# Kernel tuning notes

Measured on AMD Instinct MI355X. Metric: run time of the kernel, lower is better.

Reference implementation:

```python
import jax, jax.numpy as jnp
import numpy as np

N_NODES = 50000
N_EDGES = 800000
NC = 16
FDIM = 13
FHID = 64


def setup_inputs() -> dict:
    key = jax.random.key(0)
    ks = jax.random.split(key, 10)
    inp = {
        "hx": jax.random.normal(ks[0], (N_NODES, NC), jnp.float32),
        "edgefeats": jax.random.normal(ks[1], (N_EDGES, FDIM), jnp.float32),
        "idxn": jax.random.randint(ks[2], (N_EDGES,), 0, N_NODES, jnp.int32),
        "edge_dst": jnp.sort(jax.random.randint(ks[3], (N_EDGES,), 0, N_NODES, jnp.int32)),
        "fnet_w1": jax.random.normal(ks[4], (FDIM, FHID), jnp.float32) * 0.3,
        "fnet_b1": jnp.zeros((FHID,), jnp.float32),
        "fnet_w2": jax.random.normal(ks[5], (FHID, NC * NC), jnp.float32) * 0.05,
        "fnet_b2": jnp.zeros((NC * NC,), jnp.float32),
        "w_ih": jax.random.normal(ks[6], (3 * NC, NC), jnp.float32) * 0.25,
        "w_hh": jax.random.normal(ks[7], (3 * NC, NC), jnp.float32) * 0.25,
        "b_ih": jnp.zeros((3 * NC,), jnp.float32),
        "b_hh": jnp.zeros((3 * NC,), jnp.float32),
    }
    return inp


def _gru_cell(x, h, w_ih, w_hh, b_ih, b_hh):
    gi = x @ w_ih.T + b_ih  # [N, 3*nc]
    gh = h @ w_hh.T + b_hh
    i_r, i_z, i_n = jnp.split(gi, 3, axis=1)
    h_r, h_z, h_n = jnp.split(gh, 3, axis=1)
    r = jax.nn.sigmoid(i_r + h_r)
    z = jax.nn.sigmoid(i_z + h_z)
    n = jnp.tanh(i_n + r * h_n)
    return (1.0 - z) * n + z * h


def reference(hx, edgefeats, idxn, edge_dst, fnet_w1, fnet_b1, fnet_w2, fnet_b2,
              w_ih, w_hh, b_ih, b_hh):
    n_nodes, nc = hx.shape
    # Filter-generating network: per-edge [nc, nc] weight matrices (shared over iterations).
    w_flat = jax.nn.relu(edgefeats @ fnet_w1 + fnet_b1) @ fnet_w2 + fnet_b2
    W = w_flat.reshape(-1, nc, nc)  # [E, nc, nc]
    # Degree normalization per destination node.
    deg = jax.ops.segment_sum(jnp.ones_like(edge_dst, dtype=hx.dtype), edge_dst,
                              num_segments=n_nodes)
    inv_deg = (1.0 / jnp.maximum(deg, 1.0))[:, None]  # [N, 1]

    def gconv(h):
        msgs = jnp.einsum('ec,ecd->ed', h[idxn], W)  # gather + per-edge matmul
        agg = jax.ops.segment_sum(msgs, edge_dst, num_segments=n_nodes)
        return agg * inv_deg

    def cell(inp, h):
        return _gru_cell(inp, h, w_ih, w_hh, b_ih, b_hh)

    hxs = [hx]
    h1 = cell(gconv(hx), hx); hxs.append(h1)
    h2 = cell(gconv(h1), h1); hxs.append(h2)
    h3 = cell(gconv(h2), h2)
    s1 = h1 + h3; hxs.append(s1)
    h4 = cell(gconv(s1), s1); hxs.append(h4)
    h5 = cell(gconv(h4), h4)
    s2 = h3 + h5; hxs.append(s2)
    h6 = cell(gconv(s2), s2); hxs.append(h6)
    h7 = cell(gconv(h6), h6)
    s3 = h5 + h7; hxs.append(s3)
    h8 = cell(gconv(s3), s3); hxs.append(h8)
    h9 = cell(gconv(h8), h8)
    s4 = h7 + h9; hxs.append(s4)
    h10 = cell(gconv(s4), s4); hxs.append(h10)
    return jnp.concatenate(hxs, axis=1)  # cat_all=True -> [N, 11*nc]
```

## Files before the change

kernel.cpp:

```cpp
#include <hip/hip_runtime.h>

#define NN 50000
#define NE 800000
#define OUTC 176

typedef unsigned int uint32;
typedef short bf16x8 __attribute__((ext_vector_type(8)));
typedef float f32x4 __attribute__((ext_vector_type(4)));

__device__ __forceinline__ uint32 f2bf_rne(float f) {
  union { float f; uint32 u; } v; v.f = f;
  uint32 u = v.u;
  return (u + 0x7FFFu + ((u >> 16) & 1u)) >> 16;
}
__device__ __forceinline__ uint32 packbf2(float a, float b) {
  return f2bf_rne(a) | (f2bf_rne(b) << 16);
}
__device__ __forceinline__ float blo(uint32 u) {
  union { uint32 x; float f; } t; t.x = u << 16; return t.f;
}
__device__ __forceinline__ float bhi(uint32 u) {
  union { uint32 x; float f; } t; t.x = u & 0xFFFF0000u; return t.f;
}
__device__ __forceinline__ float bf2f(unsigned short v) {
  union { uint32 x; float f; } t; t.x = ((uint32)v) << 16; return t.f;
}
__device__ __forceinline__ float sb2f(uint32 w, int b) {
  return (float)((int)(w << (24 - 8 * b)) >> 24);
}

__global__ __launch_bounds__(256) void deg_count_kernel(const int* __restrict__ edst,
                                                        float* __restrict__ deg) {
  int e = blockIdx.x * 256 + threadIdx.x;
  if (e < NE) atomicAdd(&deg[edst[e]], 1.0f);
}

__global__ __launch_bounds__(256) void deg_inv_kernel(float* __restrict__ deg) {
  int n = blockIdx.x * 256 + threadIdx.x;
  if (n < NN) deg[n] = 1.0f / fmaxf(deg[n], 1.0f);
}

__global__ __launch_bounds__(256) void copy_col0_kernel(const float* __restrict__ hx,
                                                        float* __restrict__ out) {
  int n = blockIdx.x * 256 + threadIdx.x;
  if (n >= NN) return;
  const float4* s = reinterpret_cast<const float4*>(hx + (size_t)n * 16);
  float4* d = reinterpret_cast<float4*>(out + (size_t)n * OUTC);
  d[0] = s[0]; d[1] = s[1]; d[2] = s[2]; d[3] = s[3];
}

__global__ __launch_bounds__(256) void repack_w2_kernel(const float* __restrict__ w2,
                                                        float* __restrict__ w2t) {
  int i = blockIdx.x * 256 + threadIdx.x;
  if (i >= 256 * 1024) return;
  int d = i >> 10, r = i & 1023, k = r >> 4, c = r & 15;
  w2t[i] = w2[k * 256 + c * 16 + d];
}

__global__ __launch_bounds__(256) void repack_w2f_kernel(const float* __restrict__ w2,
                                                         unsigned short* __restrict__ w2f) {
  int i = blockIdx.x * 256 + threadIdx.x;
  if (i >= 16384) return;
  int jj = i & 7;
  int l = (i >> 3) & 63;
  int nbm = i >> 9;
  int m = nbm & 1, nb = nbm >> 1;
  int k = m * 32 + (l >> 4) * 8 + jj;
  int j = nb * 16 + (l & 15);
  w2f[i] = (unsigned short)f2bf_rne(w2[k * 256 + j]);
}

__global__ __launch_bounds__(256) void fnet_mfma_i8_kernel(
    const float* __restrict__ ef, const float* __restrict__ w1, const float* __restrict__ b1,
    const unsigned short* __restrict__ w2f, const float* __restrict__ b2,
    unsigned char* __restrict__ W, unsigned short* __restrict__ S, int wo) {
  __shared__ float efs[832];
  const int wave = threadIdx.x >> 6;
  const int l = threadIdx.x & 63;
  const int wid = wo + blockIdx.x * 4 + wave;
  const int d = l & 15, kg = l >> 4;

  long long E0 = ((long long)wo + (long long)blockIdx.x * 4) * 16;
  if (threadIdx.x < 208) {
    reinterpret_cast<float4*>(efs)[threadIdx.x] =
        reinterpret_cast<const float4*>(ef + E0 * 13)[threadIdx.x];
  }
  __syncthreads();

  const int eloc = wave * 16 + d;
  float f[13];
#pragma unroll
  for (int i = 0; i < 13; ++i) f[i] = efs[eloc * 13 + i];
  float ua[8], ub[8];
#pragma unroll
  for (int j = 0; j < 8; ++j) { ua[j] = b1[kg * 8 + j]; ub[j] = b1[32 + kg * 8 + j]; }
#pragma unroll
  for (int i = 0; i < 13; ++i) {
    const float4* wa = reinterpret_cast<const float4*>(w1 + i * 64 + kg * 8);
    const float4* wb = reinterpret_cast<const float4*>(w1 + i * 64 + 32 + kg * 8);
    float4 a0 = wa[0], a1 = wa[1], c0 = wb[0], c1 = wb[1];
    float fi = f[i];
    ua[0] = fmaf(fi, a0.x, ua[0]); ua[1] = fmaf(fi, a0.y, ua[1]);
    ua[2] = fmaf(fi, a0.z, ua[2]); ua[3] = fmaf(fi, a0.w, ua[3]);
    ua[4] = fmaf(fi, a1.x, ua[4]); ua[5] = fmaf(fi, a1.y, ua[5]);
    ua[6] = fmaf(fi, a1.z, ua[6]); ua[7] = fmaf(fi, a1.w, ua[7]);
    ub[0] = fmaf(fi, c0.x, ub[0]); ub[1] = fmaf(fi, c0.y, ub[1]);
    ub[2] = fmaf(fi, c0.z, ub[2]); ub[3] = fmaf(fi, c0.w, ub[3]);
    ub[4] = fmaf(fi, c1.x, ub[4]); ub[5] = fmaf(fi, c1.y, ub[5]);
    ub[6] = fmaf(fi, c1.z, ub[6]); ub[7] = fmaf(fi, c1.w, ub[7]);
  }
  bf16x8 afrag0, afrag1;
#pragma unroll
  for (int j = 0; j < 8; ++j) {
    afrag0[j] = (short)f2bf_rne(fmaxf(ua[j], 0.0f));
    afrag1[j] = (short)f2bf_rne(fmaxf(ub[j], 0.0f));
  }

  const bf16x8* Bp = reinterpret_cast<const bf16x8*>(w2f);
  f32x4 acc[16];
#pragma unroll
  for (int nb = 0; nb < 16; ++nb) {
    float bias = b2[nb * 16 + d];
    f32x4 c; c[0] = bias; c[1] = bias; c[2] = bias; c[3] = bias;
    bf16x8 bf0 = Bp[(nb * 2 + 0) * 64 + l];
    bf16x8 bf1 = Bp[(nb * 2 + 1) * 64 + l];
    c = __builtin_amdgcn_mfma_f32_16x16x32_bf16(afrag0, bf0, c, 0, 0, 0);
    c = __builtin_amdgcn_mfma_f32_16x16x32_bf16(afrag1, bf1, c, 0, 0, 0);
    acc[nb] = c;
  }

  float mx[4];
#pragma unroll
  for (int r = 0; r < 4; ++r) {
    float m = 0.0f;
#pragma unroll
    for (int c = 0; c < 16; ++c) m = fmaxf(m, fabsf(acc[c][r]));
    mx[r] = m;
  }
#pragma unroll
  for (int mask = 1; mask < 16; mask <<= 1) {
#pragma unroll
    for (int r = 0; r < 4; ++r) mx[r] = fmaxf(mx[r], __shfl_xor(mx[r], mask));
  }
  uint32 sb[4]; float sinv[4];
#pragma unroll
  for (int r = 0; r < 4; ++r) {
    sb[r] = f2bf_rne(mx[r] * (1.0f / 127.0f));
    float sd = bf2f((unsigned short)sb[r]);
    sinv[r] = (sd > 0.0f) ? (1.0f / sd) : 0.0f;
  }
  if (d == 0) {
    uint32 lo = sb[0] | (sb[1] << 16), hi = sb[2] | (sb[3] << 16);
    *reinterpret_cast<uint2*>(S + (size_t)wid * 16 + kg * 4) = make_uint2(lo, hi);
  }

#pragma unroll
  for (int r = 0; r < 4; ++r) {
    size_t er = (size_t)wid * 16 + kg * 4 + r;
    uint32 p[4];
#pragma unroll
    for (int q = 0; q < 4; ++q) {
      uint32 wv = 0;
#pragma unroll
      for (int b = 0; b < 4; ++b) {
        float qf = fminf(127.0f, fmaxf(-127.0f, rintf(acc[q * 4 + b][r] * sinv[r])));
        wv |= ((uint32)((int)qf & 255)) << (8 * b);
      }
      p[q] = wv;
    }
    *reinterpret_cast<uint4*>(W + (er << 8) + (d << 4)) = make_uint4(p[0], p[1], p[2], p[3]);
  }
}

__device__ __forceinline__ void fnet_layer1(const float* __restrict__ ef, long long e,
                                            const float* __restrict__ w1,
                                            const float* __restrict__ b1,
                                            float* u) {
  float f[13];
#pragma unroll
  for (int i = 0; i < 13; ++i) f[i] = ef[(size_t)e * 13 + i];
#pragma unroll
  for (int k = 0; k < 64; ++k) u[k] = b1[k];
#pragma unroll
  for (int i = 0; i < 13; ++i) {
    float fi = f[i];
#pragma unroll
    for (int k = 0; k < 64; ++k) u[k] = fmaf(fi, w1[i * 64 + k], u[k]);
  }
#pragma unroll
  for (int k = 0; k < 64; ++k) u[k] = fmaxf(u[k], 0.0f);
}

__global__ __launch_bounds__(256) void fnet_bf16_kernel(
    const float* __restrict__ ef, const float* __restrict__ w1, const float* __restrict__ b1,
    const float* __restrict__ w2t, const float* __restrict__ b2,
    unsigned short* __restrict__ W, long long ebase, int ecnt) {
  int t = blockIdx.x * 256 + threadIdx.x;
  if (t >= ecnt) return;
  float u[64];
  fnet_layer1(ef, ebase + t, w1, b1, u);
#pragma unroll 1
  for (int dt = 0; dt < 8; ++dt) {
    uint32 p[16];
#pragma unroll
    for (int dd = 0; dd < 2; ++dd) {
      const int d = dt * 2 + dd;
      const float* wr = w2t + ((size_t)d << 10);
      float acc[16];
#pragma unroll
      for (int c = 0; c < 16; ++c) acc[c] = b2[c * 16 + d];
#pragma unroll
      for (int k = 0; k < 64; ++k) {
        float uk = u[k];
#pragma unroll
        for (int c = 0; c < 16; ++c) acc[c] = fmaf(uk, wr[k * 16 + c], acc[c]);
      }
#pragma unroll
      for (int q = 0; q < 8; ++q) p[dd * 8 + q] = packbf2(acc[2 * q], acc[2 * q + 1]);
    }
    uint4* dp = reinterpret_cast<uint4*>(W + ((size_t)t << 8) + (dt << 5));
    dp[0] = make_uint4(p[0], p[1], p[2], p[3]);
    dp[1] = make_uint4(p[4], p[5], p[6], p[7]);
    dp[2] = make_uint4(p[8], p[9], p[10], p[11]);
    dp[3] = make_uint4(p[12], p[13], p[14], p[15]);
  }
}

__global__ __launch_bounds__(256) void msg_bf16_kernel(
    const float* __restrict__ h, int h_ld,
    const unsigned short* __restrict__ W, long long ebase, int ecnt,
    const int* __restrict__ idxn, const int* __restrict__ edst,
    float* __restrict__ agg) {
  int t = blockIdx.x * 256 + threadIdx.x;
  if (t >= ecnt) return;
  int g = t >> 4, d = t & 15;
  int cur = -1;
  float acc = 0.0f;
  for (int s = 0; s < 16; ++s) {
    int erel = g * 16 + s;
    long long e = ebase + erel;
    int dst = edst[e];
    if (dst != cur) {
      if (cur >= 0) atomicAdd(&agg[(size_t)cur * 16 + d], acc);
      cur = dst; acc = 0.0f;
    }
    int src = idxn[e];
    const float4* hp = reinterpret_cast<const float4*>(h + (size_t)src * h_ld);
    float4 a0 = hp[0], a1 = hp[1], a2 = hp[2], a3 = hp[3];
    const uint4* wp = reinterpret_cast<const uint4*>(W + ((size_t)erel << 8) + (d << 4));
    uint4 w0 = wp[0], w1 = wp[1];
    acc = fmaf(a0.x, blo(w0.x), acc); acc = fmaf(a0.y, bhi(w0.x), acc);
    acc = fmaf(a0.z, blo(w0.y), acc); acc = fmaf(a0.w, bhi(w0.y), acc);
    acc = fmaf(a1.x, blo(w0.z), acc); acc = fmaf(a1.y, bhi(w0.z), acc);
    acc = fmaf(a1.z, blo(w0.w), acc); acc = fmaf(a1.w, bhi(w0.w), acc);
    acc = fmaf(a2.x, blo(w1.x), acc); acc = fmaf(a2.y, bhi(w1.x), acc);
    acc = fmaf(a2.z, blo(w1.y), acc); acc = fmaf(a2.w, bhi(w1.y), acc);
    acc = fmaf(a3.x, blo(w1.z), acc); acc = fmaf(a3.y, bhi(w1.z), acc);
    acc = fmaf(a3.z, blo(w1.w), acc); acc = fmaf(a3.w, bhi(w1.w), acc);
  }
  if (cur >= 0) atomicAdd(&agg[(size_t)cur * 16 + d], acc);
}

__global__ __launch_bounds__(256) void msg_i8_kernel(
    const float* __restrict__ h, int h_ld,
    const unsigned char* __restrict__ W, const unsigned short* __restrict__ S,
    const int* __restrict__ idxn, const int* __restrict__ edst,
    float* __restrict__ agg) {
  int t = blockIdx.x * 256 + threadIdx.x;
  if (t >= NE) return;
  const int g = t >> 4, d = t & 15;
  const int base = threadIdx.x & 48;
  const int e0 = g * 16;

  int my_dst = edst[e0 + d];
  int my_src = idxn[e0 + d];

  int srcn = __shfl(my_src, base);
  const float4* hp = reinterpret_cast<const float4*>(h + (size_t)srcn * h_ld);
  float4 na0 = hp[0], na1 = hp[1], na2 = hp[2], na3 = hp[3];
  uint4 nwv = *reinterpret_cast<const uint4*>(W + ((size_t)e0 << 8) + (d << 4));
  float nsc = bf2f(S[e0]);

  int cur = -1;
  float acc = 0.0f;
#pragma unroll
  for (int s = 0; s < 16; ++s) {
    float4 a0 = na0, a1 = na1, a2 = na2, a3 = na3;
    uint4 wv = nwv;
    float sc = nsc;
    int dst = __shfl(my_dst, base + s);
    if (s < 15) {
      int sn = __shfl(my_src, base + s + 1);
      const float4* hq = reinterpret_cast<const float4*>(h + (size_t)sn * h_ld);
      na0 = hq[0]; na1 = hq[1]; na2 = hq[2]; na3 = hq[3];
      nwv = *reinterpret_cast<const uint4*>(W + ((size_t)(e0 + s + 1) << 8) + (d << 4));
      nsc = bf2f(S[e0 + s + 1]);
    }
    if (dst != cur) {
      if (cur >= 0) atomicAdd(&agg[(size_t)cur * 16 + d], acc);
      cur = dst; acc = 0.0f;
    }
    float r = 0.0f;
    r = fmaf(a0.x, sb2f(wv.x, 0), r); r = fmaf(a0.y, sb2f(wv.x, 1), r);
    r = fmaf(a0.z, sb2f(wv.x, 2), r); r = fmaf(a0.w, sb2f(wv.x, 3), r);
    r = fmaf(a1.x, sb2f(wv.y, 0), r); r = fmaf(a1.y, sb2f(wv.y, 1), r);
    r = fmaf(a1.z, sb2f(wv.y, 2), r); r = fmaf(a1.w, sb2f(wv.y, 3), r);
    r = fmaf(a2.x, sb2f(wv.z, 0), r); r = fmaf(a2.y, sb2f(wv.z, 1), r);
    r = fmaf(a2.z, sb2f(wv.z, 2), r); r = fmaf(a2.w, sb2f(wv.z, 3), r);
    r = fmaf(a3.x, sb2f(wv.w, 0), r); r = fmaf(a3.y, sb2f(wv.w, 1), r);
    r = fmaf(a3.z, sb2f(wv.w, 2), r); r = fmaf(a3.w, sb2f(wv.w, 3), r);
    acc = fmaf(r, sc, acc);
  }
  atomicAdd(&agg[(size_t)cur * 16 + d], acc);
}

__global__ __launch_bounds__(256) void cell_kernel(
    const float* __restrict__ agg, const float* __restrict__ invd,
    const float* hin, int hin_ld,
    const float* __restrict__ wih, const float* __restrict__ whh,
    const float* __restrict__ bih, const float* __restrict__ bhh,
    float* hout, int hout_ld,
    const float* sprev, int sprev_ld,
    float* sout, int sout_ld,
    float* hdn) {
  int t = blockIdx.x * 256 + threadIdx.x;
  int n = t >> 4, j = t & 15;
  if (n >= NN) return;
  float inv = invd[n];
  float x[16], h[16];
  const float4* ap = reinterpret_cast<const float4*>(agg + (size_t)n * 16);
  const float4* hp = reinterpret_cast<const float4*>(hin + (size_t)n * hin_ld);
#pragma unroll
  for (int q = 0; q < 4; ++q) {
    float4 a = ap[q];
    x[4 * q + 0] = a.x * inv; x[4 * q + 1] = a.y * inv;
    x[4 * q + 2] = a.z * inv; x[4 * q + 3] = a.w * inv;
    float4 hv4 = hp[q];
    h[4 * q + 0] = hv4.x; h[4 * q + 1] = hv4.y;
    h[4 * q + 2] = hv4.z; h[4 * q + 3] = hv4.w;
  }
  const float4* wr4 = reinterpret_cast<const float4*>(wih + j * 16);
  const float4* wz4 = reinterpret_cast<const float4*>(wih + (16 + j) * 16);
  const float4* wn4 = reinterpret_cast<const float4*>(wih + (32 + j) * 16);
  const float4* vr4 = reinterpret_cast<const float4*>(whh + j * 16);
  const float4* vz4 = reinterpret_cast<const float4*>(whh + (16 + j) * 16);
  const float4* vn4 = reinterpret_cast<const float4*>(whh + (32 + j) * 16);
  float gr = bih[j], gz = bih[16 + j], gn = bih[32 + j];
  float hr = bhh[j], hz = bhh[16 + j], hn = bhh[32 + j];
#pragma unroll
  for (int q = 0; q < 4; ++q) {
    float4 wr = wr4[q], wz = wz4[q], wn = wn4[q];
    float4 vr = vr4[q], vz = vz4[q], vn = vn4[q];
    gr = fmaf(x[4 * q + 0], wr.x, gr); gr = fmaf(x[4 * q + 1], wr.y, gr);
    gr = fmaf(x[4 * q + 2], wr.z, gr); gr = fmaf(x[4 * q + 3], wr.w, gr);
    gz = fmaf(x[4 * q + 0], wz.x, gz); gz = fmaf(x[4 * q + 1], wz.y, gz);
    gz = fmaf(x[4 * q + 2], wz.z, gz); gz = fmaf(x[4 * q + 3], wz.w, gz);
    gn = fmaf(x[4 * q + 0], wn.x, gn); gn = fmaf(x[4 * q + 1], wn.y, gn);
    gn = fmaf(x[4 * q + 2], wn.z, gn); gn = fmaf(x[4 * q + 3], wn.w, gn);
    hr = fmaf(h[4 * q + 0], vr.x, hr); hr = fmaf(h[4 * q + 1], vr.y, hr);
    hr = fmaf(h[4 * q + 2], vr.z, hr); hr = fmaf(h[4 * q + 3], vr.w, hr);
    hz = fmaf(h[4 * q + 0], vz.x, hz); hz = fmaf(h[4 * q + 1], vz.y, hz);
    hz = fmaf(h[4 * q + 2], vz.z, hz); hz = fmaf(h[4 * q + 3], vz.w, hz);
    hn = fmaf(h[4 * q + 0], vn.x, hn); hn = fmaf(h[4 * q + 1], vn.y, hn);
    hn = fmaf(h[4 * q + 2], vn.z, hn); hn = fmaf(h[4 * q + 3], vn.w, hn);
  }
  float r = 1.0f / (1.0f + expf(-(gr + hr)));
  float z = 1.0f / (1.0f + expf(-(gz + hz)));
  float nng = tanhf(gn + r * hn);
  float hv = (1.0f - z) * nng + z * h[j];

  bool do_s = (sprev != nullptr);
  float sv = 0.0f;
  if (do_s) sv = hv + sprev[(size_t)n * sprev_ld + j];
  hout[(size_t)n * hout_ld + j] = hv;
  if (do_s) sout[(size_t)n * sout_ld + j] = sv;
  if (hdn != nullptr) hdn[(size_t)n * 16 + j] = do_s ? sv : hv;
}

extern "C" void kernel_launch(void* const* d_in, const int* in_sizes, int n_in,
                              void* d_out, int out_size, void* d_ws, size_t ws_size,
                              hipStream_t stream) {
  const float* hx   = (const float*)d_in[0];
  const float* ef   = (const float*)d_in[1];
  const int*   idxn = (const int*)d_in[2];
  const int*   edst = (const int*)d_in[3];
  const float* w1   = (const float*)d_in[4];
  const float* b1   = (const float*)d_in[5];
  const float* w2   = (const float*)d_in[6];
  const float* b2   = (const float*)d_in[7];
  const float* wih  = (const float*)d_in[8];
  const float* whh  = (const float*)d_in[9];
  const float* bih  = (const float*)d_in[10];
  const float* bhh  = (const float*)d_in[11];
  float* out = (float*)d_out;

  const size_t INV_OFF = 0;
  const size_t AGG_OFF = 200064;
  const size_t W2T_OFF = 3400192;
  const size_t HD_OFF  = W2T_OFF + 1048576;
  const size_t W_OFF   = HD_OFF + (size_t)NN * 64;
  if (ws_size < W_OFF + 1600 * 512) return;
  char* wsb = (char*)d_ws;
  float* invd = (float*)(wsb + INV_OFF);
  float* agg  = (float*)(wsb + AGG_OFF);
  float* w2t  = (float*)(wsb + W2T_OFF);
  unsigned short* w2f = (unsigned short*)(wsb + W2T_OFF);
  float* hd   = (float*)(wsb + HD_OFF);
  unsigned short* W16 = (unsigned short*)(wsb + W_OFF);
  unsigned char*  W8  = (unsigned char*)(wsb + W_OFF);
  unsigned short* S16 = (unsigned short*)(wsb + W_OFF + (size_t)NE * 256);
  size_t wrem = ws_size - W_OFF;

  int plan;
  size_t chunk = NE;
  if (wrem >= (size_t)NE * 260) plan = 1;
  else {
    plan = 2;
    chunk = (wrem / 512) & ~(size_t)15;
    if (chunk > NE) chunk = NE;
  }

  const int NB  = (NN + 255) / 256;
  const int EB  = (NE + 255) / 256;
  const int CB  = (NN * 16 + 255) / 256;

  hipMemsetAsync(invd, 0, (size_t)NN * 4, stream);
  deg_count_kernel<<<EB, 256, 0, stream>>>(edst, invd);
  deg_inv_kernel<<<NB, 256, 0, stream>>>(invd);
  copy_col0_kernel<<<NB, 256, 0, stream>>>(hx, out);

  if (plan == 1) {
    repack_w2f_kernel<<<64, 256, 0, stream>>>(w2, w2f);
    for (int c = 0; c < 4; ++c)
      fnet_mfma_i8_kernel<<<3125, 256, 0, stream>>>(ef, w1, b1, w2f, b2, W8, S16,
                                                    c * 12500);
  } else {
    repack_w2_kernel<<<1024, 256, 0, stream>>>(w2, w2t);
  }

  auto col = [&](int c) { return out + (size_t)c * 16; };

  auto step = [&](const float* hin, int hin_ld, float* hout,
                  const float* sprev, float* sout, float* hdn) {
    hipMemsetAsync(agg, 0, (size_t)NN * 64, stream);
    if (plan == 1) {
      msg_i8_kernel<<<EB, 256, 0, stream>>>(hin, hin_ld, W8, S16, idxn, edst, agg);
    } else {
      for (size_t e0 = 0; e0 < NE; e0 += chunk) {
        int cnt = (int)(((size_t)NE - e0) < chunk ? ((size_t)NE - e0) : chunk);
        fnet_bf16_kernel<<<(cnt + 255) / 256, 256, 0, stream>>>(ef, w1, b1, w2t, b2, W16,
                                                                (long long)e0, cnt);
        msg_bf16_kernel<<<(cnt + 255) / 256, 256, 0, stream>>>(hin, hin_ld, W16,
                                                               (long long)e0, cnt,
                                                               idxn, edst, agg);
      }
    }
    cell_kernel<<<CB, 256, 0, stream>>>(agg, invd, hin, hin_ld, wih, whh, bih, bhh,
                                        hout, OUTC, sprev, OUTC, sout, OUTC, hdn);
  };

  step(hx, 16, col(1),  nullptr, nullptr, hd);
  step(hd, 16, col(2),  nullptr, nullptr, hd);
  step(hd, 16, col(10), col(1),  col(3),  hd);
  step(hd, 16, col(4),  nullptr, nullptr, hd);
  step(hd, 16, col(10), col(10), col(5),  hd);
  step(hd, 16, col(6),  nullptr, nullptr, hd);
  step(hd, 16, col(10), col(10), col(7),  hd);
  step(hd, 16, col(8),  nullptr, nullptr, hd);
  step(hd, 16, col(10), col(10), col(9),  hd);
  step(hd, 16, col(10), nullptr, nullptr, nullptr);
}
```

Measured before the change: 1.001 ms.

## Process two edge groups per thread in message kernel and stage w2 in LDS

The message kernel now has each 16-lane group handle two 16-edge runs interleaved, so half as many threads are launched and each thread keeps two independent gather/accumulate chains in flight. The shuffle-based software prefetch of the next edge is replaced by direct per-iteration loads of edst/idxn. Separately, the filter-network kernel copies the repacked w2 (32 KB) into shared memory per block and hoists bias loads. The LDS copy adds per-block load cost and LDS pressure that may cut occupancy, and halving the thread count may reduce latency hiding in the gather-bound message step.

```diff
diff --git a/kernel.cpp b/kernel.cpp
--- a/kernel.cpp
+++ b/kernel.cpp
@@ -75,11 +75,16 @@
     const unsigned short* __restrict__ w2f, const float* __restrict__ b2,
     unsigned char* __restrict__ W, unsigned short* __restrict__ S, int wo) {
   __shared__ float efs[832];
+  __shared__ short w2s[16384];
   const int wave = threadIdx.x >> 6;
   const int l = threadIdx.x & 63;
   const int wid = wo + blockIdx.x * 4 + wave;
   const int d = l & 15, kg = l >> 4;
 
+#pragma unroll
+  for (int i = 0; i < 8; ++i)
+    reinterpret_cast<uint4*>(w2s)[threadIdx.x + 256 * i] =
+        reinterpret_cast<const uint4*>(w2f)[threadIdx.x + 256 * i];
   long long E0 = ((long long)wo + (long long)blockIdx.x * 4) * 16;
   if (threadIdx.x < 208) {
     reinterpret_cast<float4*>(efs)[threadIdx.x] =
@@ -116,12 +121,15 @@
     afrag1[j] = (short)f2bf_rne(fmaxf(ub[j], 0.0f));
   }
 
-  const bf16x8* Bp = reinterpret_cast<const bf16x8*>(w2f);
+  float bias[16];
+#pragma unroll
+  for (int nb = 0; nb < 16; ++nb) bias[nb] = b2[nb * 16 + d];
+
+  const bf16x8* Bp = reinterpret_cast<const bf16x8*>(w2s);
   f32x4 acc[16];
 #pragma unroll
   for (int nb = 0; nb < 16; ++nb) {
-    float bias = b2[nb * 16 + d];
-    f32x4 c; c[0] = bias; c[1] = bias; c[2] = bias; c[3] = bias;
+    f32x4 c; c[0] = bias[nb]; c[1] = bias[nb]; c[2] = bias[nb]; c[3] = bias[nb];
     bf16x8 bf0 = Bp[(nb * 2 + 0) * 64 + l];
     bf16x8 bf1 = Bp[(nb * 2 + 1) * 64 + l];
     c = __builtin_amdgcn_mfma_f32_16x16x32_bf16(afrag0, bf0, c, 0, 0, 0);
@@ -261,57 +269,59 @@
   if (cur >= 0) atomicAdd(&agg[(size_t)cur * 16 + d], acc);
 }
 
+__device__ __forceinline__ float edge_dot_i8(const float4& a0, const float4& a1,
+                                             const float4& a2, const float4& a3,
+                                             const uint4& wv) {
+  float r = 0.0f;
+  r = fmaf(a0.x, sb2f(wv.x, 0), r); r = fmaf(a0.y, sb2f(wv.x, 1), r);
+  r = fmaf(a0.z, sb2f(wv.x, 2), r); r = fmaf(a0.w, sb2f(wv.x, 3), r);
+  r = fmaf(a1.x, sb2f(wv.y, 0), r); r = fmaf(a1.y, sb2f(wv.y, 1), r);
+  r = fmaf(a1.z, sb2f(wv.y, 2), r); r = fmaf(a1.w, sb2f(wv.y, 3), r);
+  r = fmaf(a2.x, sb2f(wv.z, 0), r); r = fmaf(a2.y, sb2f(wv.z, 1), r);
+  r = fmaf(a2.z, sb2f(wv.z, 2), r); r = fmaf(a2.w, sb2f(wv.z, 3), r);
+  r = fmaf(a3.x, sb2f(wv.w, 0), r); r = fmaf(a3.y, sb2f(wv.w, 1), r);
+  r = fmaf(a3.z, sb2f(wv.w, 2), r); r = fmaf(a3.w, sb2f(wv.w, 3), r);
+  return r;
+}
+
 __global__ __launch_bounds__(256) void msg_i8_kernel(
     const float* __restrict__ h, int h_ld,
     const unsigned char* __restrict__ W, const unsigned short* __restrict__ S,
     const int* __restrict__ idxn, const int* __restrict__ edst,
     float* __restrict__ agg) {
   int t = blockIdx.x * 256 + threadIdx.x;
-  if (t >= NE) return;
+  if (t >= NE / 2) return;
   const int g = t >> 4, d = t & 15;
-  const int base = threadIdx.x & 48;
-  const int e0 = g * 16;
-
-  int my_dst = edst[e0 + d];
-  int my_src = idxn[e0 + d];
-
-  int srcn = __shfl(my_src, base);
-  const float4* hp = reinterpret_cast<const float4*>(h + (size_t)srcn * h_ld);
-  float4 na0 = hp[0], na1 = hp[1], na2 = hp[2], na3 = hp[3];
-  uint4 nwv = *reinterpret_cast<const uint4*>(W + ((size_t)e0 << 8) + (d << 4));
-  float nsc = bf2f(S[e0]);
-
-  int cur = -1;
-  float acc = 0.0f;
+  const int eA0 = g * 32;
+  const int eB0 = g * 32 + 16;
+
+  int curA = -1, curB = -1;
+  float accA = 0.0f, accB = 0.0f;
 #pragma unroll
   for (int s = 0; s < 16; ++s) {
-    float4 a0 = na0, a1 = na1, a2 = na2, a3 = na3;
-    uint4 wv = nwv;
-    float sc = nsc;
-    int dst = __shfl(my_dst, base + s);
-    if (s < 15) {
-      int sn = __shfl(my_src, base + s + 1);
-      const float4* hq = reinterpret_cast<const float4*>(h + (size_t)sn * h_ld);
-      na0 = hq[0]; na1 = hq[1]; na2 = hq[2]; na3 = hq[3];
-      nwv = *reinterpret_cast<const uint4*>(W + ((size_t)(e0 + s + 1) << 8) + (d << 4));
-      nsc = bf2f(S[e0 + s + 1]);
-    }
-    if (dst != cur) {
-      if (cur >= 0) atomicAdd(&agg[(size_t)cur * 16 + d], acc);
-      cur = dst; acc = 0.0f;
-    }
-    float r = 0.0f;
-    r = fmaf(a0.x, sb2f(wv.x, 0), r); r = fmaf(a0.y, sb2f(wv.x, 1), r);
-    r = fmaf(a0.z, sb2f(wv.x, 2), r); r = fmaf(a0.w, sb2f(wv.x, 3), r);
-    r = fmaf(a1.x, sb2f(wv.y, 0), r); r = fmaf(a1.y, sb2f(wv.y, 1), r);
-    r = fmaf(a1.z, sb2f(wv.y, 2), r); r = fmaf(a1.w, sb2f(wv.y, 3), r);
-    r = fmaf(a2.x, sb2f(wv.z, 0), r); r = fmaf(a2.y, sb2f(wv.z, 1), r);
-    r = fmaf(a2.z, sb2f(wv.z, 2), r); r = fmaf(a2.w, sb2f(wv.z, 3), r);
-    r = fmaf(a3.x, sb2f(wv.w, 0), r); r = fmaf(a3.y, sb2f(wv.w, 1), r);
-    r = fmaf(a3.z, sb2f(wv.w, 2), r); r = fmaf(a3.w, sb2f(wv.w, 3), r);
-    acc = fmaf(r, sc, acc);
-  }
-  atomicAdd(&agg[(size_t)cur * 16 + d], acc);
+    int eA = eA0 + s, eB = eB0 + s;
+    int dstA = edst[eA], dstB = edst[eB];
+    int srcA = idxn[eA], srcB = idxn[eB];
+    const float4* hpA = reinterpret_cast<const float4*>(h + (size_t)srcA * h_ld);
+    const float4* hpB = reinterpret_cast<const float4*>(h + (size_t)srcB * h_ld);
+    float4 a0 = hpA[0], a1 = hpA[1], a2 = hpA[2], a3 = hpA[3];
+    float4 b0 = hpB[0], b1 = hpB[1], b2 = hpB[2], b3 = hpB[3];
+    uint4 wvA = *reinterpret_cast<const uint4*>(W + ((size_t)eA << 8) + (d << 4));
+    uint4 wvB = *reinterpret_cast<const uint4*>(W + ((size_t)eB << 8) + (d << 4));
+    float scA = bf2f(S[eA]), scB = bf2f(S[eB]);
+    if (dstA != curA) {
+      if (curA >= 0) atomicAdd(&agg[(size_t)curA * 16 + d], accA);
+      curA = dstA; accA = 0.0f;
+    }
+    if (dstB != curB) {
+      if (curB >= 0) atomicAdd(&agg[(size_t)curB * 16 + d], accB);
+      curB = dstB; accB = 0.0f;
+    }
+    accA = fmaf(edge_dot_i8(a0, a1, a2, a3, wvA), scA, accA);
+    accB = fmaf(edge_dot_i8(b0, b1, b2, b3, wvB), scB, accB);
+  }
+  atomicAdd(&agg[(size_t)curA * 16 + d], accA);
+  atomicAdd(&agg[(size_t)curB * 16 + d], accB);
 }
 
 __global__ __launch_bounds__(256) void cell_kernel(
@@ -422,6 +432,7 @@
 
   const int NB  = (NN + 255) / 256;
   const int EB  = (NE + 255) / 256;
+  const int MB  = (NE / 2 + 255) / 256;
   const int CB  = (NN * 16 + 255) / 256;
 
   hipMemsetAsync(invd, 0, (size_t)NN * 4, stream);
@@ -444,7 +455,7 @@
                   const float* sprev, float* sout, float* hdn) {
     hipMemsetAsync(agg, 0, (size_t)NN * 64, stream);
     if (plan == 1) {
-      msg_i8_kernel<<<EB, 256, 0, stream>>>(hin, hin_ld, W8, S16, idxn, edst, agg);
+      msg_i8_kernel<<<MB, 256, 0, stream>>>(hin, hin_ld, W8, S16, idxn, edst, agg);
     } else {
       for (size_t e0 = 0; e0 < NE; e0 += chunk) {
         int cnt = (int)(((size_t)NE - e0) < chunk ? ((size_t)NE - e0) : chunk);
```

Measured after the change: 988.3 us. Within noise of the previous version (-1.2%).
